# Performance work log

Hardware: AMD Instinct MI355X
Metric: run time of the kernel (lower is better)

Reference implementation:

```python
import jax, jax.numpy as jnp
import numpy as np

NSTEPS = 8  # scaling-and-squaring steps
SHAPE = (2, 3, 160, 192, 160)  # (batch, ndim, D, H, W)


def _pull3d_wrap(img, coords):
    """Trilinear grid_pull with 'dft' (circular) bound, extrapolate=False.

    img:    (B, D, H, W, C) values
    coords: (B, D, H, W, 3) sampling coordinates in voxels (z, y, x order)
    """
    B, D, H, W, C = img.shape
    c0 = jnp.floor(coords)
    f = coords - c0                       # fractional part, differentiable
    c0 = c0.astype(jnp.int32)
    img_flat = img.reshape(B, D * H * W, C)
    out = jnp.zeros_like(img)
    for dz in (0, 1):
        wz = f[..., 0] if dz else (1.0 - f[..., 0])
        z = jnp.mod(c0[..., 0] + dz, D)
        for dy in (0, 1):
            wy = f[..., 1] if dy else (1.0 - f[..., 1])
            y = jnp.mod(c0[..., 1] + dy, H)
            for dx in (0, 1):
                wx = f[..., 2] if dx else (1.0 - f[..., 2])
                x = jnp.mod(c0[..., 2] + dx, W)
                idx = (z * H + y) * W + x          # (B, D, H, W)
                vals = jnp.take_along_axis(img_flat, idx.reshape(B, -1, 1), axis=1)
                vals = vals.reshape(B, D, H, W, C)
                out = out + vals * (wz * wy * wx)[..., None]
    # extrapolate=False: zero where sample lies outside voxel centers [0, n-1]
    nmax = jnp.asarray([D - 1, H - 1, W - 1], dtype=coords.dtype)
    inb = jnp.all((coords >= 0.0) & (coords <= nmax), axis=-1)
    return jnp.where(inb[..., None], out, 0.0)


def setup_inputs() -> dict:
    key = jax.random.key(0)
    flow = jax.random.normal(key, SHAPE, dtype=jnp.float32)
    return {"flow": flow}


def reference(flow) -> jnp.ndarray:
    """FlowExp forward (interpolation='linear', bound='dft', extrapolate=False,
    coeff=False). Linear spline coefficients == values, so ValueToCoeff /
    CoeffToValue are identities and the loop is pure composition:
        v <- grid_pull(v, identity_grid + v)
    """
    v = jnp.moveaxis(flow, 1, -1) / (2 ** NSTEPS)   # (B, D, H, W, 3)
    B, D, H, W, _ = v.shape
    gz, gy, gx = jnp.meshgrid(
        jnp.arange(D, dtype=v.dtype),
        jnp.arange(H, dtype=v.dtype),
        jnp.arange(W, dtype=v.dtype),
        indexing="ij",
    )
    grid = jnp.stack([gz, gy, gx], axis=-1)          # identity grid (D,H,W,3)
    for _ in range(NSTEPS):
        v = _pull3d_wrap(v, grid[None] + v)
    return jnp.moveaxis(v, -1, 1)                    # (B, 3, D, H, W)
```

## Files before the change

kernel.cpp:

```cpp
#include <hip/hip_runtime.h>


#define BB 2
#define DD 160
#define HH 192
#define WW 160

constexpr int HW    = HH * WW;
constexpr int PLANE = DD * HW;
constexpr int TX = 32, TY = 8, TZ = 8;
constexpr int SX = TX + 2, SY = TY + 2, SZ = TZ + 2;
constexpr int SYX  = SY * SX;
constexpr int SLICE   = 3 * SYX;
constexpr int SLICE_P = 1024;
constexpr int LDSF = SZ * SLICE_P;

constexpr int GX = WW / TX;
constexpr int GY = HH / TY;
constexpr int GZ = (DD / TZ) * BB;
constexpr int NBLK  = GX * GY * GZ;
constexpr int CHUNK = NBLK / 8;

__device__ __forceinline__ void gld_lds4(const float* g, float* l) {
    __builtin_amdgcn_global_load_lds(
        (const __attribute__((address_space(1))) void*)g,
        (__attribute__((address_space(3))) void*)l, 4, 0, 0);
}

__device__ __forceinline__ void tile_coords(int& x0, int& y0, int& z0, int& b) {
    const int lid = blockIdx.x + GX * (blockIdx.y + GY * blockIdx.z);
    const int nl  = (lid & 7) * CHUNK + (lid >> 3);
    const int bx  = nl % GX;
    int r = nl / GX;
    const int by  = r % GY;
    r /= GY;
    b  = r / (DD / TZ);
    x0 = bx * TX;
    y0 = by * TY;
    z0 = (r % (DD / TZ)) * TZ;
}

__device__ __forceinline__ int row_term(int syi, int sxi, int x0, int y0,
                                        bool border) {
    if (!border) return (y0 - 1 + syi) * WW + (x0 - 1 + sxi);
    const int gy = min(max(y0 - 1 + syi, 0), HH - 1);
    const int gx = min(max(x0 - 1 + sxi, 0), WW - 1);
    return gy * WW + gx;
}

__global__ __launch_bounds__(256, 4) void flow_first(const float* __restrict__ vin,
                                                     float* __restrict__ vout,
                                                     float scale) {
    __shared__ float lds[LDSF];
    const int tid = threadIdx.x;
    int x0, y0, z0, b;
    tile_coords(x0, y0, z0, b);
    const bool border = (x0 == 0) | (x0 + TX >= WW) |
                        (y0 == 0) | (y0 + TY >= HH) |
                        (z0 == 0) | (z0 + TZ >= DD);
    const float* vb = vin + b * 3 * PLANE;

    int g0, g1, g2, g3;
    {
        const int l0 = tid;
        int c = l0 / SYX, r = l0 - c * SYX, a = r / SX;
        g0 = c * PLANE + row_term(a, r - a * SX, x0, y0, border);
        const int l1 = tid + 256;
        c = l1 / SYX; r = l1 - c * SYX; a = r / SX;
        g1 = c * PLANE + row_term(a, r - a * SX, x0, y0, border);
        const int l2 = tid + 512;
        c = l2 / SYX; r = l2 - c * SYX; a = r / SX;
        g2 = c * PLANE + row_term(a, r - a * SX, x0, y0, border);
        const int l3 = min(tid + 768, SLICE - 1);
        c = l3 / SYX; r = l3 - c * SYX; a = r / SX;
        g3 = c * PLANE + row_term(a, r - a * SX, x0, y0, border);
    }

    #pragma unroll
    for (int szi = 0; szi < SZ; ++szi) {
        int zb = z0 - 1 + szi;
        if (border) zb = min(max(zb, 0), DD - 1);
        const float* sp = vb + zb * HW;
        float* lb = lds + szi * SLICE_P;
        gld_lds4(sp + g0, lb + tid);
        gld_lds4(sp + g1, lb + tid + 256);
        gld_lds4(sp + g2, lb + tid + 512);
        gld_lds4(sp + g3, lb + tid + 768);
    }
    __syncthreads();

    const int tx = tid & (TX - 1), ty = tid >> 5;
    const int x = x0 + tx, y = y0 + ty;
    #pragma unroll 2
    for (int zz = 0; zz < TZ; ++zz) {
        const int z = z0 + zz;
        const int so = (zz + 1) * SLICE_P + (ty + 1) * SX + (tx + 1);
        const float vz = lds[so] * scale;
        const float vy = lds[so + SYX] * scale;
        const float vx = lds[so + 2 * SYX] * scale;
        const float cz = (float)z + vz, cy = (float)y + vy, cx = (float)x + vx;
        const bool jz = vz < 0.f, jy = vy < 0.f, jx = vx < 0.f;
        const float gzf = jz ? vz + 1.f : vz;
        const float gyf = jy ? vy + 1.f : vy;
        const float gxf = jx ? vx + 1.f : vx;
        const bool inb = (cz >= 0.f) & (cz <= (float)(DD - 1)) &
                         (cy >= 0.f) & (cy <= (float)(HH - 1)) &
                         (cx >= 0.f) & (cx <= (float)(WW - 1));
        const float m = inb ? 1.f : 0.f;
        const float wz1 = gzf * m, wz0 = m - wz1;
        const float wy1 = gyf, wy0 = 1.f - gyf;
        const float wx1 = gxf, wx0 = 1.f - gxf;
        const int sb = ((so - (jx ? 1 : 0)) - (jy ? SX : 0))
                       - (jz ? SLICE_P : 0);
        float oz = 0.f, oy = 0.f, ox = 0.f;
        #pragma unroll
        for (int dz = 0; dz < 2; ++dz) {
            const float wzv = dz ? wz1 : wz0;
            #pragma unroll
            for (int dy = 0; dy < 2; ++dy) {
                const float wzy = wzv * (dy ? wy1 : wy0);
                const float w0 = wzy * wx0, w1 = wzy * wx1;
                const int o = sb + dz * SLICE_P + dy * SX;
                oz += lds[o] * w0;
                oy += lds[o + SYX] * w0;
                ox += lds[o + 2 * SYX] * w0;
                oz += lds[o + 1] * w1;
                oy += lds[o + SYX + 1] * w1;
                ox += lds[o + 2 * SYX + 1] * w1;
            }
        }
        float t[3] = { oz * scale, oy * scale, ox * scale };
        __builtin_memcpy(vout + (((b * DD + z) * HH + y) * WW + x) * 3, t, 12);
    }
}

template<int OUT_PLANAR>
__global__ __launch_bounds__(256, 4) void flow_mid(const float* __restrict__ vin,
                                                   float* __restrict__ vout) {
    __shared__ float lds[LDSF];
    const int tid = threadIdx.x;
    int x0, y0, z0, b;
    tile_coords(x0, y0, z0, b);
    const bool border = (x0 == 0) | (x0 + TX >= WW) |
                        (y0 == 0) | (y0 + TY >= HH) |
                        (z0 == 0) | (z0 + TZ >= DD);
    const float* vb = vin + b * PLANE * 3;

    int g0, g1, g2, g3;
    {
        const int l0 = tid;
        int v = l0 / 3, c = l0 - v * 3, a = v / SX;
        g0 = row_term(a, v - a * SX, x0, y0, border) * 3 + c;
        const int l1 = tid + 256;
        v = l1 / 3; c = l1 - v * 3; a = v / SX;
        g1 = row_term(a, v - a * SX, x0, y0, border) * 3 + c;
        const int l2 = tid + 512;
        v = l2 / 3; c = l2 - v * 3; a = v / SX;
        g2 = row_term(a, v - a * SX, x0, y0, border) * 3 + c;
        const int l3 = min(tid + 768, SLICE - 1);
        v = l3 / 3; c = l3 - v * 3; a = v / SX;
        g3 = row_term(a, v - a * SX, x0, y0, border) * 3 + c;
    }

    #pragma unroll
    for (int szi = 0; szi < SZ; ++szi) {
        int zb = z0 - 1 + szi;
        if (border) zb = min(max(zb, 0), DD - 1);
        const float* sp = vb + zb * (HW * 3);
        float* lb = lds + szi * SLICE_P;
        gld_lds4(sp + g0, lb + tid);
        gld_lds4(sp + g1, lb + tid + 256);
        gld_lds4(sp + g2, lb + tid + 512);
        gld_lds4(sp + g3, lb + tid + 768);
    }
    __syncthreads();

    const int tx = tid & (TX - 1), ty = tid >> 5;
    const int x = x0 + tx, y = y0 + ty;
    #pragma unroll 2
    for (int zz = 0; zz < TZ; ++zz) {
        const int z = z0 + zz;
        const int so = (zz + 1) * SLICE_P + 3 * ((ty + 1) * SX + (tx + 1));
        const float vz = lds[so], vy = lds[so + 1], vx = lds[so + 2];
        const float cz = (float)z + vz, cy = (float)y + vy, cx = (float)x + vx;
        const bool jz = vz < 0.f, jy = vy < 0.f, jx = vx < 0.f;
        const float gzf = jz ? vz + 1.f : vz;
        const float gyf = jy ? vy + 1.f : vy;
        const float gxf = jx ? vx + 1.f : vx;
        const bool inb = (cz >= 0.f) & (cz <= (float)(DD - 1)) &
                         (cy >= 0.f) & (cy <= (float)(HH - 1)) &
                         (cx >= 0.f) & (cx <= (float)(WW - 1));
        const float m = inb ? 1.f : 0.f;
        const float wz1 = gzf * m, wz0 = m - wz1;
        const float wy1 = gyf, wy0 = 1.f - gyf;
        const float wx1 = gxf, wx0 = 1.f - gxf;
        const int sb = ((so - (jx ? 3 : 0)) - (jy ? 3 * SX : 0))
                       - (jz ? SLICE_P : 0);
        float oz = 0.f, oy = 0.f, ox = 0.f;
        #pragma unroll
        for (int dz = 0; dz < 2; ++dz) {
            const float wzv = dz ? wz1 : wz0;
            #pragma unroll
            for (int dy = 0; dy < 2; ++dy) {
                const float wzy = wzv * (dy ? wy1 : wy0);
                const float w0 = wzy * wx0, w1 = wzy * wx1;
                const int o = sb + dz * SLICE_P + dy * (3 * SX);
                oz += lds[o]     * w0; oy += lds[o + 1] * w0; ox += lds[o + 2] * w0;
                oz += lds[o + 3] * w1; oy += lds[o + 4] * w1; ox += lds[o + 5] * w1;
            }
        }
        if (OUT_PLANAR) {
            float* op = vout + b * 3 * PLANE + (z * HH + y) * WW + x;
            op[0] = oz; op[PLANE] = oy; op[2 * PLANE] = ox;
        } else {
            float t[3] = { oz, oy, ox };
            __builtin_memcpy(vout + (((b * DD + z) * HH + y) * WW + x) * 3, t, 12);
        }
    }
}

extern "C" void kernel_launch(void* const* d_in, const int* in_sizes, int n_in,
                              void* d_out, int out_size, void* d_ws, size_t ws_size,
                              hipStream_t stream) {
    const float* flow = (const float*)d_in[0];
    float* out = (float*)d_out;
    float* wsA = (float*)d_ws;

    dim3 blk(256);
    dim3 grd(GX, GY, GZ);
    const float s = 1.f / 256.f;

    flow_first<<<grd, blk, 0, stream>>>(flow, wsA, s);
    flow_mid<0><<<grd, blk, 0, stream>>>(wsA, out);
    flow_mid<0><<<grd, blk, 0, stream>>>(out, wsA);
    flow_mid<0><<<grd, blk, 0, stream>>>(wsA, out);
    flow_mid<0><<<grd, blk, 0, stream>>>(out, wsA);
    flow_mid<0><<<grd, blk, 0, stream>>>(wsA, out);
    flow_mid<0><<<grd, blk, 0, stream>>>(out, wsA);
    flow_mid<1><<<grd, blk, 0, stream>>>(wsA, out);
}
```

Measured before the change: 385.9 us.

## Split LDS halo wait into two phases to overlap gathers with loads

After: 393.5 us. About the same (+2.0%).

```diff
diff --git a/kernel.cpp b/kernel.cpp
--- a/kernel.cpp
+++ b/kernel.cpp
@@ -173,48 +173,71 @@
         gld_lds4(sp + g2, lb + tid + 512);
         gld_lds4(sp + g3, lb + tid + 768);
     }
-    __syncthreads();
 
     const int tx = tid & (TX - 1), ty = tid >> 5;
     const int x = x0 + tx, y = y0 + ty;
-    #pragma unroll 2
+    float res[TZ][3];
+
+#define GATHER_Z(zz)                                                          \
+    {                                                                         \
+        const int z = z0 + (zz);                                              \
+        const int so = ((zz) + 1) * SLICE_P + 3 * ((ty + 1) * SX + (tx + 1)); \
+        const float vz = lds[so], vy = lds[so + 1], vx = lds[so + 2];         \
+        const float cz = (float)z + vz, cy = (float)y + vy,                   \
+                    cx = (float)x + vx;                                       \
+        const bool jz = vz < 0.f, jy = vy < 0.f, jx = vx < 0.f;               \
+        const float gzf = jz ? vz + 1.f : vz;                                 \
+        const float gyf = jy ? vy + 1.f : vy;                                 \
+        const float gxf = jx ? vx + 1.f : vx;                                 \
+        const bool inb = (cz >= 0.f) & (cz <= (float)(DD - 1)) &              \
+                         (cy >= 0.f) & (cy <= (float)(HH - 1)) &              \
+                         (cx >= 0.f) & (cx <= (float)(WW - 1));               \
+        const float m = inb ? 1.f : 0.f;                                      \
+        const float wz1 = gzf * m, wz0 = m - wz1;                             \
+        const float wy1 = gyf, wy0 = 1.f - gyf;                               \
+        const float wx1 = gxf, wx0 = 1.f - gxf;                               \
+        const int sb = ((so - (jx ? 3 : 0)) - (jy ? 3 * SX : 0))              \
+                       - (jz ? SLICE_P : 0);                                  \
+        float oz = 0.f, oy = 0.f, ox = 0.f;                                   \
+        _Pragma("unroll")                                                     \
+        for (int dz = 0; dz < 2; ++dz) {                                      \
+            const float wzv = dz ? wz1 : wz0;                                 \
+            _Pragma("unroll")                                                 \
+            for (int dy = 0; dy < 2; ++dy) {                                  \
+                const float wzy = wzv * (dy ? wy1 : wy0);                     \
+                const float w0 = wzy * wx0, w1 = wzy * wx1;                   \
+                const int o = sb + dz * SLICE_P + dy * (3 * SX);              \
+                oz += lds[o]     * w0; oy += lds[o + 1] * w0;                 \
+                ox += lds[o + 2] * w0;                                        \
+                oz += lds[o + 3] * w1; oy += lds[o + 4] * w1;                 \
+                ox += lds[o + 5] * w1;                                        \
+            }                                                                 \
+        }                                                                     \
+        res[zz][0] = oz; res[zz][1] = oy; res[zz][2] = ox;                    \
+    }
+
+    asm volatile("s_waitcnt vmcnt(16)" ::: "memory");
+    __builtin_amdgcn_sched_barrier(0);
+    __builtin_amdgcn_s_barrier();
+    __builtin_amdgcn_sched_barrier(0);
+    GATHER_Z(0) GATHER_Z(1) GATHER_Z(2) GATHER_Z(3)
+
+    asm volatile("s_waitcnt vmcnt(0)" ::: "memory");
+    __builtin_amdgcn_sched_barrier(0);
+    __builtin_amdgcn_s_barrier();
+    __builtin_amdgcn_sched_barrier(0);
+    GATHER_Z(4) GATHER_Z(5) GATHER_Z(6) GATHER_Z(7)
+#undef GATHER_Z
+
+    #pragma unroll
     for (int zz = 0; zz < TZ; ++zz) {
         const int z = z0 + zz;
-        const int so = (zz + 1) * SLICE_P + 3 * ((ty + 1) * SX + (tx + 1));
-        const float vz = lds[so], vy = lds[so + 1], vx = lds[so + 2];
-        const float cz = (float)z + vz, cy = (float)y + vy, cx = (float)x + vx;
-        const bool jz = vz < 0.f, jy = vy < 0.f, jx = vx < 0.f;
-        const float gzf = jz ? vz + 1.f : vz;
-        const float gyf = jy ? vy + 1.f : vy;
-        const float gxf = jx ? vx + 1.f : vx;
-        const bool inb = (cz >= 0.f) & (cz <= (float)(DD - 1)) &
-                         (cy >= 0.f) & (cy <= (float)(HH - 1)) &
-                         (cx >= 0.f) & (cx <= (float)(WW - 1));
-        const float m = inb ? 1.f : 0.f;
-        const float wz1 = gzf * m, wz0 = m - wz1;
-        const float wy1 = gyf, wy0 = 1.f - gyf;
-        const float wx1 = gxf, wx0 = 1.f - gxf;
-        const int sb = ((so - (jx ? 3 : 0)) - (jy ? 3 * SX : 0))
-                       - (jz ? SLICE_P : 0);
-        float oz = 0.f, oy = 0.f, ox = 0.f;
-        #pragma unroll
-        for (int dz = 0; dz < 2; ++dz) {
-            const float wzv = dz ? wz1 : wz0;
-            #pragma unroll
-            for (int dy = 0; dy < 2; ++dy) {
-                const float wzy = wzv * (dy ? wy1 : wy0);
-                const float w0 = wzy * wx0, w1 = wzy * wx1;
-                const int o = sb + dz * SLICE_P + dy * (3 * SX);
-                oz += lds[o]     * w0; oy += lds[o + 1] * w0; ox += lds[o + 2] * w0;
-                oz += lds[o + 3] * w1; oy += lds[o + 4] * w1; ox += lds[o + 5] * w1;
-            }
-        }
         if (OUT_PLANAR) {
             float* op = vout + b * 3 * PLANE + (z * HH + y) * WW + x;
-            op[0] = oz; op[PLANE] = oy; op[2 * PLANE] = ox;
+            op[0] = res[zz][0]; op[PLANE] = res[zz][1]; op[2 * PLANE] = res[zz][2];
         } else {
-            float t[3] = { oz, oy, ox };
-            __builtin_memcpy(vout + (((b * DD + z) * HH + y) * WW + x) * 3, t, 12);
+            __builtin_memcpy(vout + (((b * DD + z) * HH + y) * WW + x) * 3,
+                             res[zz], 12);
         }
     }
 }
```
